# Performance work log

Hardware: AMD Instinct MI355X
Metric: run time of the kernel (lower is better)

## Reference

```python
import jax, jax.numpy as jnp
import numpy as np

STEPS = 50   # MattingSolver(steps=50)
H, W = 1024, 1024
EPS = 1e-2   # diagonal regularization (matting lambda-like), guarantees SPD


def _build_laplacian():
    """5-point weighted graph Laplacian + EPS*I on an HxW grid, COO, row-sorted."""
    rng = np.random.RandomState(0)
    n = H * W
    idx = np.arange(n, dtype=np.int32).reshape(H, W)
    wh = rng.rand(H, W - 1).astype(np.float32) + 0.1  # horizontal edge weights
    wv = rng.rand(H - 1, W).astype(np.float32) + 0.1  # vertical edge weights
    a_h, b_h = idx[:, :-1].ravel(), idx[:, 1:].ravel()
    a_v, b_v = idx[:-1, :].ravel(), idx[1:, :].ravel()
    diag_idx = np.arange(n, dtype=np.int32)
    rows = np.concatenate([a_h, b_h, a_v, b_v, diag_idx])
    cols = np.concatenate([b_h, a_h, b_v, a_v, diag_idx])
    off = np.concatenate([wh.ravel(), wh.ravel(), wv.ravel(), wv.ravel()])
    deg = np.zeros(n, dtype=np.float32)
    np.add.at(deg, a_h, wh.ravel()); np.add.at(deg, b_h, wh.ravel())
    np.add.at(deg, a_v, wv.ravel()); np.add.at(deg, b_v, wv.ravel())
    vals = np.concatenate([-off, deg + EPS]).astype(np.float32)
    order = np.argsort(rows, kind='stable')
    return rows[order], cols[order], vals[order]


def setup_inputs() -> dict:
    key = jax.random.key(0)
    rows, cols, vals = _build_laplacian()
    b = jax.random.normal(key, (H * W,), dtype=jnp.float32)
    return {"rows": jnp.asarray(rows), "cols": jnp.asarray(cols),
            "vals": jnp.asarray(vals), "b": b}


def reference(rows, cols, vals, b):
    """Unpreconditioned conjugate gradient: solve A x = b, x0 = 0, STEPS iters."""
    n = b.shape[0]

    def spmv(p):  # y = A @ p via COO gather + segment-sum scatter
        return jax.ops.segment_sum(vals * p[cols], rows, num_segments=n,
                                   indices_are_sorted=True)

    x0 = jnp.zeros_like(b)
    r0 = b                      # r = b - A @ 0
    rs0 = jnp.dot(r0, r0)

    def body(carry, _):
        x, r, p, rs = carry
        Ap = spmv(p)
        alpha = rs / jnp.dot(p, Ap)
        x = x + alpha * p
        r = r - alpha * Ap
        rs_new = jnp.dot(r, r)
        p = r + (rs_new / rs) * p
        return (x, r, p, rs_new), None

    (x, _, _, _), _ = jax.lax.scan(body, (x0, r0, r0, rs0), None, length=STEPS)
    return x
```

## Files before the change

### kernel.cpp

```cpp
#include <hip/hip_runtime.h>

#define HH 1024
#define WW 1024
#define CG_STEPS 50
#define NB 256
#define NT 1024

#define SCOPE __HIP_MEMORY_SCOPE_AGENT
#define POISON64 0xAAAAAAAAAAAAAAAAULL

__device__ __forceinline__ float aload(const float* p) {
    return __hip_atomic_load(p, __ATOMIC_RELAXED, SCOPE);
}
__device__ __forceinline__ void astore(float* p, float v) {
    __hip_atomic_store(p, v, __ATOMIC_RELAXED, SCOPE);
}
__device__ __forceinline__ int iload(const int* p) {
    return __hip_atomic_load(p, __ATOMIC_RELAXED, SCOPE);
}
__device__ __forceinline__ void istore(int* p, int v) {
    __hip_atomic_store(p, v, __ATOMIC_RELAXED, SCOPE);
}
__device__ __forceinline__ unsigned long long uload(const unsigned long long* p) {
    return __hip_atomic_load(p, __ATOMIC_RELAXED, SCOPE);
}
__device__ __forceinline__ void ustore(unsigned long long* p, unsigned long long v) {
    __hip_atomic_store(p, v, __ATOMIC_RELAXED, SCOPE);
}

__global__ __launch_bounds__(NT)
void cgsolve_kernel(const int* __restrict__ cols, const float* __restrict__ vals,
                    const float* __restrict__ b, float* __restrict__ xout,
                    float* __restrict__ rbuf, unsigned long long* __restrict__ red,
                    int* __restrict__ flags) {
    const int col = threadIdx.x;
    const int bb  = blockIdx.x;

    __shared__ float sr[4][WW + 1];
    __shared__ float sa[16], sb[16];
    __shared__ float sg1, sg2;
    __shared__ int   scols[2][5 * WW];
    __shared__ float svals[2][5 * WW];

    float adiag[4], art[4], alf[4], adn[4], awu[4];
    float x_[4], r_[4], w_[4], q_[4];
    float p_[4] = {0.f, 0.f, 0.f, 0.f};
    float s_[4] = {0.f, 0.f, 0.f, 0.f};
    float z_[4] = {0.f, 0.f, 0.f, 0.f};

    for (int half = 0; half < 2; ++half) {
        __syncthreads();
        #pragma unroll
        for (int rr2 = 0; rr2 < 2; ++rr2) {
            const int i    = 4 * bb + 2 * half + rr2;
            const int off  = (i == 0) ? 0 : (4 * WW - 2) + (i - 1) * (5 * WW - 2);
            const int base = 1 + (i > 0) + (i < HH - 1);
            const int len2 = (base * WW + 2 * WW - 2) >> 1;
            const int2*   gc = (const int2*)(cols + off);
            const float2* gv = (const float2*)(vals + off);
            int2*   lc = (int2*)scols[rr2];
            float2* lv = (float2*)svals[rr2];
            for (int e = threadIdx.x; e < len2; e += NT) {
                lc[e] = gc[e];
                lv[e] = gv[e];
            }
        }
        __syncthreads();
        #pragma unroll
        for (int rr2 = 0; rr2 < 2; ++rr2) {
            const int rr     = 2 * half + rr2;
            const int i      = 4 * bb + rr;
            const int base   = 1 + (i > 0) + (i < HH - 1);
            const int j      = col;
            const int within = (j == 0) ? 0 : (base + 1) + (j - 1) * (base + 2);
            const int nnz    = base + (j > 0) + (j < WW - 1);
            const int t      = i * WW + j;
            float dg = 0.f, wr = 0.f, wl = 0.f, wd = 0.f, wu = 0.f;
            #pragma unroll
            for (int e = 0; e < 5; ++e) {
                if (e < nnz) {
                    const int   c = scols[rr2][within + e];
                    const float v = svals[rr2][within + e];
                    if (c == t)           dg = v;
                    else if (c == t + 1)  wr = v;
                    else if (c == t - 1)  wl = v;
                    else if (c == t + WW) wd = v;
                    else if (c == t - WW) wu = v;
                }
            }
            adiag[rr] = dg; art[rr] = wr; alf[rr] = wl; adn[rr] = wd; awu[rr] = wu;
            r_[rr] = b[t];
            x_[rr] = 0.f;
        }
    }

    auto consumeRed = [&](int k, float& o1, float& o2) {
        if (threadIdx.x < 64) {
            const int lane = threadIdx.x;
            const unsigned long long* basep = red + (size_t)k * NB;
            unsigned long long v[4];
            #pragma unroll
            for (int m = 0; m < 4; ++m) v[m] = uload(basep + m * 64 + lane);
            while (v[0] == POISON64 || v[1] == POISON64 ||
                   v[2] == POISON64 || v[3] == POISON64) {
                __builtin_amdgcn_s_sleep(1);
                #pragma unroll
                for (int m = 0; m < 4; ++m)
                    if (v[m] == POISON64) v[m] = uload(basep + m * 64 + lane);
            }
            float a = 0.f, bb2 = 0.f;
            #pragma unroll
            for (int m = 0; m < 4; ++m) {
                a   += __uint_as_float((unsigned)(v[m] & 0xFFFFFFFFu));
                bb2 += __uint_as_float((unsigned)(v[m] >> 32));
            }
            #pragma unroll
            for (int mask = 1; mask < 64; mask <<= 1) {
                a   += __shfl_xor(a,   mask, 64);
                bb2 += __shfl_xor(bb2, mask, 64);
            }
            if (lane == 0) { sg1 = a; sg2 = bb2; }
        }
        __syncthreads();
        o1 = sg1; o2 = sg2;
    };

    auto blockPartialPost = [&](int k, float a, float bfl, int flagval) {
        #pragma unroll
        for (int mask = 1; mask < 64; mask <<= 1) {
            a   += __shfl_xor(a,   mask, 64);
            bfl += __shfl_xor(bfl, mask, 64);
        }
        const int lane = threadIdx.x & 63, wid = threadIdx.x >> 6;
        if (lane == 0) { sa[wid] = a; sb[wid] = bfl; }
        __syncthreads();
        if (threadIdx.x < 16) {
            float ta = sa[threadIdx.x], tb = sb[threadIdx.x];
            #pragma unroll
            for (int mask = 1; mask < 16; mask <<= 1) {
                ta += __shfl_xor(ta, mask, 16);
                tb += __shfl_xor(tb, mask, 16);
            }
            if (threadIdx.x == 0) {
                const unsigned long long v =
                    ((unsigned long long)__float_as_uint(tb) << 32) |
                    (unsigned long long)__float_as_uint(ta);
                ustore(&red[(size_t)k * NB + bb], v);
                istore(&flags[bb], flagval);
            }
        }
    };

    {
        #pragma unroll
        for (int rr = 0; rr < 4; ++rr) sr[rr][col] = r_[rr];
        __syncthreads();
        const float btop = (bb > 0)      ? b[(4 * bb - 1) * WW + col] : 0.f;
        const float bbot = (bb < NB - 1) ? b[(4 * bb + 4) * WW + col] : 0.f;
        float rs_l = 0.f, dl_l = 0.f;
        #pragma unroll
        for (int rr = 0; rr < 4; ++rr) {
            float sum = adiag[rr] * r_[rr];
            const float vr = (col < WW - 1) ? sr[rr][col + 1] : 0.f;
            const float vl = (col > 0)      ? sr[rr][col - 1] : 0.f;
            sum += art[rr] * vr + alf[rr] * vl;
            const float vd = (rr < 3) ? r_[rr + 1] : bbot;
            const float vu = (rr > 0) ? r_[rr - 1] : btop;
            sum += adn[rr] * vd + awu[rr] * vu;
            w_[rr] = sum;
            rs_l += r_[rr] * r_[rr];
            dl_l += sum * r_[rr];
        }
        astore(&rbuf[(2 * bb + 0) * WW + col], w_[0]);
        astore(&rbuf[(2 * bb + 1) * WW + col], w_[3]);
        blockPartialPost(0, rs_l, dl_l, 1);
    }

    float gamma_prev = 1.f, alpha_prev = 1.f;

    #pragma unroll 1
    for (int k = 0; k < CG_STEPS; ++k) {
        if (k < CG_STEPS - 1) {
            #pragma unroll
            for (int rr = 0; rr < 4; ++rr) sr[rr][col] = w_[rr];
            if (threadIdx.x == 0 && bb > 0)
                while (iload(&flags[bb - 1]) < k + 1) __builtin_amdgcn_s_sleep(1);
            if (threadIdx.x == 1 && bb < NB - 1)
                while (iload(&flags[bb + 1]) < k + 1) __builtin_amdgcn_s_sleep(1);
            __syncthreads();
            const float* hb = rbuf + (size_t)(k & 1) * 2 * NB * WW;
            const float wtop = (bb > 0)
                ? aload(&hb[(2 * (bb - 1) + 1) * WW + col]) : 0.f;
            const float wbot = (bb < NB - 1)
                ? aload(&hb[(2 * (bb + 1) + 0) * WW + col]) : 0.f;
            #pragma unroll
            for (int rr = 0; rr < 4; ++rr) {
                float sum = adiag[rr] * w_[rr];
                const float vr = (col < WW - 1) ? sr[rr][col + 1] : 0.f;
                const float vl = (col > 0)      ? sr[rr][col - 1] : 0.f;
                sum += art[rr] * vr + alf[rr] * vl;
                const float vd = (rr < 3) ? w_[rr + 1] : wbot;
                const float vu = (rr > 0) ? w_[rr - 1] : wtop;
                sum += adn[rr] * vd + awu[rr] * vu;
                q_[rr] = sum;
            }
        }

        float gam, del;
        consumeRed(k, gam, del);

        const float beta  = (k == 0) ? 0.f : gam / gamma_prev;
        const float alpha = (k == 0) ? gam / del
                                     : gam / (del - beta * gam / alpha_prev);
        #pragma unroll
        for (int rr = 0; rr < 4; ++rr) {
            p_[rr] = r_[rr] + beta * p_[rr];
            x_[rr] += alpha * p_[rr];
        }
        if (k == CG_STEPS - 1) break;

        float rs_l = 0.f, dl_l = 0.f;
        #pragma unroll
        for (int rr = 0; rr < 4; ++rr) {
            z_[rr] = q_[rr] + beta * z_[rr];
            s_[rr] = w_[rr] + beta * s_[rr];
            r_[rr] -= alpha * s_[rr];
            w_[rr] -= alpha * z_[rr];
            rs_l += r_[rr] * r_[rr];
            dl_l += w_[rr] * r_[rr];
        }
        float* hbn = rbuf + (size_t)((k + 1) & 1) * 2 * NB * WW;
        astore(&hbn[(2 * bb + 0) * WW + col], w_[0]);
        astore(&hbn[(2 * bb + 1) * WW + col], w_[3]);
        blockPartialPost(k + 1, rs_l, dl_l, k + 2);

        gamma_prev = gam; alpha_prev = alpha;
    }

    #pragma unroll
    for (int rr = 0; rr < 4; ++rr)
        xout[(4 * bb + rr) * WW + col] = x_[rr];
}

extern "C" void kernel_launch(void* const* d_in, const int* in_sizes, int n_in,
                              void* d_out, int out_size, void* d_ws, size_t ws_size,
                              hipStream_t stream) {
    const int*   cols = (const int*)d_in[1];
    const float* vals = (const float*)d_in[2];
    const float* b    = (const float*)d_in[3];
    float* x = (float*)d_out;

    float* w    = (float*)d_ws;
    float* rbuf = w;
    unsigned long long* red =
        (unsigned long long*)(rbuf + 2 * 2 * (size_t)NB * WW);
    int* flags = (int*)(red + (size_t)CG_STEPS * NB);

    cgsolve_kernel<<<dim3(NB), dim3(NT), 0, stream>>>(cols, vals, b, x,
                                                      rbuf, red, flags);
}
```

Before: 259.8 us.

## Use tagged double-precision reduction ring instead of poison-initialized per-step slots

Replaces the per-step float reduction slots, which relied on a poison-filled workspace, with a 4-entry ring of 64-bit words. Each word holds an iteration tag plus a truncated double partial sum. Partial sums and scalar recurrences move to double precision, and the global read is spread over 256 threads instead of 64 threads reading 4 slots each. The aim is to stop depending on a pre-poisoned workspace and to gain accuracy. The cost is more FP64 shuffles and doubled store traffic per block, and the ring is only safe if no block runs more than a few steps ahead of the others.

```diff
diff --git a/kernel.cpp b/kernel.cpp
--- a/kernel.cpp
+++ b/kernel.cpp
@@ -1,13 +1,14 @@
 #include <hip/hip_runtime.h>
+
 
 #define HH 1024
 #define WW 1024
 #define CG_STEPS 50
 #define NB 256
 #define NT 1024
+#define RING 4
 
 #define SCOPE __HIP_MEMORY_SCOPE_AGENT
-#define POISON64 0xAAAAAAAAAAAAAAAAULL
 
 __device__ __forceinline__ float aload(const float* p) {
     return __hip_atomic_load(p, __ATOMIC_RELAXED, SCOPE);
@@ -26,21 +27,30 @@
 }
 __device__ __forceinline__ void ustore(unsigned long long* p, unsigned long long v) {
     __hip_atomic_store(p, v, __ATOMIC_RELAXED, SCOPE);
+}
+
+__device__ __forceinline__ unsigned long long packtd(unsigned tag, double d) {
+    return ((unsigned long long)tag << 48) |
+           (((unsigned long long)__double_as_longlong(d)) >> 16);
+}
+__device__ __forceinline__ double unpacktd(unsigned long long v) {
+    return __longlong_as_double((long long)(v << 16));
 }
 
 __global__ __launch_bounds__(NT)
 void cgsolve_kernel(const int* __restrict__ cols, const float* __restrict__ vals,
                     const float* __restrict__ b, float* __restrict__ xout,
-                    float* __restrict__ rbuf, unsigned long long* __restrict__ red,
+                    float* __restrict__ rbuf,
+                    unsigned long long* __restrict__ redr,
                     int* __restrict__ flags) {
     const int col = threadIdx.x;
     const int bb  = blockIdx.x;
 
-    __shared__ float sr[4][WW + 1];
-    __shared__ float sa[16], sb[16];
-    __shared__ float sg1, sg2;
-    __shared__ int   scols[2][5 * WW];
-    __shared__ float svals[2][5 * WW];
+    __shared__ float  sr[4][WW + 1];
+    __shared__ double sa[16][2];
+    __shared__ double sc[4][2];
+    __shared__ int    scols[2][5 * WW];
+    __shared__ float  svals[2][5 * WW];
 
     float adiag[4], art[4], alf[4], adn[4], awu[4];
     float x_[4], r_[4], w_[4], q_[4];
@@ -94,70 +104,13 @@
         }
     }
 
-    auto consumeRed = [&](int k, float& o1, float& o2) {
-        if (threadIdx.x < 64) {
-            const int lane = threadIdx.x;
-            const unsigned long long* basep = red + (size_t)k * NB;
-            unsigned long long v[4];
-            #pragma unroll
-            for (int m = 0; m < 4; ++m) v[m] = uload(basep + m * 64 + lane);
-            while (v[0] == POISON64 || v[1] == POISON64 ||
-                   v[2] == POISON64 || v[3] == POISON64) {
-                __builtin_amdgcn_s_sleep(1);
-                #pragma unroll
-                for (int m = 0; m < 4; ++m)
-                    if (v[m] == POISON64) v[m] = uload(basep + m * 64 + lane);
-            }
-            float a = 0.f, bb2 = 0.f;
-            #pragma unroll
-            for (int m = 0; m < 4; ++m) {
-                a   += __uint_as_float((unsigned)(v[m] & 0xFFFFFFFFu));
-                bb2 += __uint_as_float((unsigned)(v[m] >> 32));
-            }
-            #pragma unroll
-            for (int mask = 1; mask < 64; mask <<= 1) {
-                a   += __shfl_xor(a,   mask, 64);
-                bb2 += __shfl_xor(bb2, mask, 64);
-            }
-            if (lane == 0) { sg1 = a; sg2 = bb2; }
-        }
-        __syncthreads();
-        o1 = sg1; o2 = sg2;
-    };
-
-    auto blockPartialPost = [&](int k, float a, float bfl, int flagval) {
-        #pragma unroll
-        for (int mask = 1; mask < 64; mask <<= 1) {
-            a   += __shfl_xor(a,   mask, 64);
-            bfl += __shfl_xor(bfl, mask, 64);
-        }
-        const int lane = threadIdx.x & 63, wid = threadIdx.x >> 6;
-        if (lane == 0) { sa[wid] = a; sb[wid] = bfl; }
-        __syncthreads();
-        if (threadIdx.x < 16) {
-            float ta = sa[threadIdx.x], tb = sb[threadIdx.x];
-            #pragma unroll
-            for (int mask = 1; mask < 16; mask <<= 1) {
-                ta += __shfl_xor(ta, mask, 16);
-                tb += __shfl_xor(tb, mask, 16);
-            }
-            if (threadIdx.x == 0) {
-                const unsigned long long v =
-                    ((unsigned long long)__float_as_uint(tb) << 32) |
-                    (unsigned long long)__float_as_uint(ta);
-                ustore(&red[(size_t)k * NB + bb], v);
-                istore(&flags[bb], flagval);
-            }
-        }
-    };
-
     {
         #pragma unroll
         for (int rr = 0; rr < 4; ++rr) sr[rr][col] = r_[rr];
         __syncthreads();
         const float btop = (bb > 0)      ? b[(4 * bb - 1) * WW + col] : 0.f;
         const float bbot = (bb < NB - 1) ? b[(4 * bb + 4) * WW + col] : 0.f;
-        float rs_l = 0.f, dl_l = 0.f;
+        double rs_d = 0.0, dl_d = 0.0;
         #pragma unroll
         for (int rr = 0; rr < 4; ++rr) {
             float sum = adiag[rr] * r_[rr];
@@ -168,25 +121,47 @@
             const float vu = (rr > 0) ? r_[rr - 1] : btop;
             sum += adn[rr] * vd + awu[rr] * vu;
             w_[rr] = sum;
-            rs_l += r_[rr] * r_[rr];
-            dl_l += sum * r_[rr];
+            rs_d += (double)r_[rr] * r_[rr];
+            dl_d += (double)sum * r_[rr];
         }
         astore(&rbuf[(2 * bb + 0) * WW + col], w_[0]);
         astore(&rbuf[(2 * bb + 1) * WW + col], w_[3]);
-        blockPartialPost(0, rs_l, dl_l, 1);
+        #pragma unroll
+        for (int mask = 1; mask < 64; mask <<= 1) {
+            rs_d += __shfl_xor(rs_d, mask, 64);
+            dl_d += __shfl_xor(dl_d, mask, 64);
+        }
+        const int lane = threadIdx.x & 63, wid = threadIdx.x >> 6;
+        if (lane == 0) { sa[wid][0] = rs_d; sa[wid][1] = dl_d; }
+        __syncthreads();
+        if (threadIdx.x < 16) {
+            double t0 = sa[threadIdx.x][0], t1 = sa[threadIdx.x][1];
+            #pragma unroll
+            for (int mask = 1; mask < 16; mask <<= 1) {
+                t0 += __shfl_xor(t0, mask, 16);
+                t1 += __shfl_xor(t1, mask, 16);
+            }
+            if (threadIdx.x == 0) {
+                unsigned long long* bp = redr + bb;
+                ustore(bp,      packtd(0u, t0));
+                ustore(bp + NB, packtd(0u, t1));
+                istore(&flags[bb], 1);
+            }
+        }
     }
 
-    float gamma_prev = 1.f, alpha_prev = 1.f;
+    double gamma_prev = 1.0, alpha_prev = 1.0;
 
     #pragma unroll 1
     for (int k = 0; k < CG_STEPS; ++k) {
         if (k < CG_STEPS - 1) {
             #pragma unroll
             for (int rr = 0; rr < 4; ++rr) sr[rr][col] = w_[rr];
-            if (threadIdx.x == 0 && bb > 0)
-                while (iload(&flags[bb - 1]) < k + 1) __builtin_amdgcn_s_sleep(1);
-            if (threadIdx.x == 1 && bb < NB - 1)
-                while (iload(&flags[bb + 1]) < k + 1) __builtin_amdgcn_s_sleep(1);
+            if (threadIdx.x < 2) {
+                const int nb2 = bb + (threadIdx.x ? 1 : -1);
+                if (nb2 >= 0 && nb2 < NB)
+                    while (iload(&flags[nb2]) < k + 1) __builtin_amdgcn_s_sleep(1);
+            }
             __syncthreads();
             const float* hb = rbuf + (size_t)(k & 1) * 2 * NB * WW;
             const float wtop = (bb > 0)
@@ -206,33 +181,83 @@
             }
         }
 
-        float gam, del;
-        consumeRed(k, gam, del);
-
-        const float beta  = (k == 0) ? 0.f : gam / gamma_prev;
-        const float alpha = (k == 0) ? gam / del
-                                     : gam / (del - beta * gam / alpha_prev);
+        double gam, del;
+        {
+            if (threadIdx.x < NB) {
+                const unsigned want = (unsigned)k;
+                const unsigned long long* bp =
+                    redr + (size_t)(k & (RING - 1)) * 2 * NB + threadIdx.x;
+                unsigned long long v0 = uload(bp);
+                unsigned long long v1 = uload(bp + NB);
+                while ((unsigned)(v0 >> 48) != want ||
+                       (unsigned)(v1 >> 48) != want) {
+                    __builtin_amdgcn_s_sleep(1);
+                    if ((unsigned)(v0 >> 48) != want) v0 = uload(bp);
+                    if ((unsigned)(v1 >> 48) != want) v1 = uload(bp + NB);
+                }
+                double t0 = unpacktd(v0), t1 = unpacktd(v1);
+                #pragma unroll
+                for (int mask = 1; mask < 64; mask <<= 1) {
+                    t0 += __shfl_xor(t0, mask, 64);
+                    t1 += __shfl_xor(t1, mask, 64);
+                }
+                if ((threadIdx.x & 63) == 0) {
+                    const int g = threadIdx.x >> 6;
+                    sc[g][0] = t0; sc[g][1] = t1;
+                }
+            }
+            __syncthreads();
+            gam = ((sc[0][0] + sc[1][0]) + sc[2][0]) + sc[3][0];
+            del = ((sc[0][1] + sc[1][1]) + sc[2][1]) + sc[3][1];
+        }
+
+        const double beta  = (k == 0) ? 0.0 : gam / gamma_prev;
+        const double alpha = (k == 0) ? gam / del
+                                      : gam / (del - beta * gam / alpha_prev);
+        const float betaf = (float)beta, alphaf = (float)alpha;
         #pragma unroll
         for (int rr = 0; rr < 4; ++rr) {
-            p_[rr] = r_[rr] + beta * p_[rr];
-            x_[rr] += alpha * p_[rr];
+            p_[rr] = r_[rr] + betaf * p_[rr];
+            x_[rr] += alphaf * p_[rr];
         }
         if (k == CG_STEPS - 1) break;
 
-        float rs_l = 0.f, dl_l = 0.f;
+        double rs_d = 0.0, dl_d = 0.0;
         #pragma unroll
         for (int rr = 0; rr < 4; ++rr) {
-            z_[rr] = q_[rr] + beta * z_[rr];
-            s_[rr] = w_[rr] + beta * s_[rr];
-            r_[rr] -= alpha * s_[rr];
-            w_[rr] -= alpha * z_[rr];
-            rs_l += r_[rr] * r_[rr];
-            dl_l += w_[rr] * r_[rr];
+            z_[rr] = q_[rr] + betaf * z_[rr];
+            s_[rr] = w_[rr] + betaf * s_[rr];
+            r_[rr] -= alphaf * s_[rr];
+            w_[rr] -= alphaf * z_[rr];
+            rs_d += (double)r_[rr] * r_[rr];
+            dl_d += (double)w_[rr] * r_[rr];
         }
         float* hbn = rbuf + (size_t)((k + 1) & 1) * 2 * NB * WW;
         astore(&hbn[(2 * bb + 0) * WW + col], w_[0]);
         astore(&hbn[(2 * bb + 1) * WW + col], w_[3]);
-        blockPartialPost(k + 1, rs_l, dl_l, k + 2);
+        #pragma unroll
+        for (int mask = 1; mask < 64; mask <<= 1) {
+            rs_d += __shfl_xor(rs_d, mask, 64);
+            dl_d += __shfl_xor(dl_d, mask, 64);
+        }
+        const int lane = threadIdx.x & 63, wid = threadIdx.x >> 6;
+        if (lane == 0) { sa[wid][0] = rs_d; sa[wid][1] = dl_d; }
+        __syncthreads();
+        if (threadIdx.x < 16) {
+            double t0 = sa[threadIdx.x][0], t1 = sa[threadIdx.x][1];
+            #pragma unroll
+            for (int mask = 1; mask < 16; mask <<= 1) {
+                t0 += __shfl_xor(t0, mask, 16);
+                t1 += __shfl_xor(t1, mask, 16);
+            }
+            if (threadIdx.x == 0) {
+                unsigned long long* bp =
+                    redr + (size_t)((k + 1) & (RING - 1)) * 2 * NB + bb;
+                ustore(bp,      packtd((unsigned)(k + 1), t0));
+                ustore(bp + NB, packtd((unsigned)(k + 1), t1));
+                istore(&flags[bb], k + 2);
+            }
+        }
 
         gamma_prev = gam; alpha_prev = alpha;
     }
@@ -250,12 +275,11 @@
     const float* b    = (const float*)d_in[3];
     float* x = (float*)d_out;
 
-    float* w    = (float*)d_ws;
-    float* rbuf = w;
-    unsigned long long* red =
+    float* rbuf = (float*)d_ws;
+    unsigned long long* redr =
         (unsigned long long*)(rbuf + 2 * 2 * (size_t)NB * WW);
-    int* flags = (int*)(red + (size_t)CG_STEPS * NB);
+    int* flags = (int*)(redr + (size_t)RING * 2 * NB);
 
     cgsolve_kernel<<<dim3(NB), dim3(NT), 0, stream>>>(cols, vals, b, x,
-                                                      rbuf, red, flags);
-}
+                                                      rbuf, redr, flags);
+}
```

After: 287.1 us. 1.11x slower.
